# Optimization experiments

Measured on AMD Instinct MI355X. Metric: run time of the kernel, lower is better.

Reference implementation:

```python
import jax, jax.numpy as jnp
import numpy as np

BETA = 0.25  # commitment loss coefficient


def setup_inputs() -> dict:
    key = jax.random.key(0)
    kx, kc = jax.random.split(key)
    # x: [B, T, D] latents; codebooks: [M, K, D] (equal K per level -> stacked)
    x = jax.random.normal(kx, (64, 1024, 256), dtype=jnp.float32)
    # small init akin to RandomUniform(-1/K, 1/K)
    codebooks = jax.random.normal(kc, (4, 1024, 256), dtype=jnp.float32) * (1.0 / 1024.0)
    return {"x": x, "codebooks": codebooks}


def reference(x, codebooks):
    """Residual VQ forward (inference path: no EMA state update).

    Returns (y, commit_loss): y = x + stop_grad(sum_l q_l - x) (straight-through),
    commit_loss = beta * sum_l mean((stop_grad(q_l) - r_l)^2).
    """
    D = x.shape[-1]
    M = codebooks.shape[0]
    flat = x.reshape(-1, D)                      # [N, D]
    residual = flat
    q_sum = jnp.zeros_like(flat)
    commit = jnp.zeros((), dtype=x.dtype)
    for lvl in range(M):                         # M is small & fixed (4)
        cb = codebooks[lvl]                      # [K, D]
        # squared L2 distances: ||r||^2 + ||e||^2 - 2 r.e^T
        r2 = jnp.sum(residual * residual, axis=1, keepdims=True)   # [N, 1]
        e2 = jnp.sum(cb * cb, axis=1)                               # [K]
        dist = r2 + e2 - 2.0 * jnp.matmul(residual, cb.T)           # [N, K]
        idx = jnp.argmin(dist, axis=1)                              # [N]
        q = jnp.take(cb, idx, axis=0)                               # [N, D]
        q_st = jax.lax.stop_gradient(q)
        commit = commit + BETA * jnp.mean((q_st - residual) ** 2)
        q_sum = q_sum + q
        residual = residual - q_st
    y_flat = flat + jax.lax.stop_gradient(q_sum - flat)
    return y_flat.reshape(x.shape), commit
```

## Files before the change

kernel.cpp:

```cpp
#include <hip/hip_runtime.h>

#define DIM 256
#define KCODES 1024
#define LEVELS 4
#define CHUNK 64
#define NCHUNK 16
#define TOKB 128
#define NTOK 65536
#define NELEM (NTOK * DIM)

typedef _Float16 h8 __attribute__((ext_vector_type(8)));
typedef _Float16 h4 __attribute__((ext_vector_type(4)));
typedef _Float16 h2 __attribute__((ext_vector_type(2)));
typedef float f4 __attribute__((ext_vector_type(4)));
typedef unsigned int u32;

__device__ __forceinline__ void gload16(const void* g, void* l) {
  __builtin_amdgcn_global_load_lds(
      (const __attribute__((address_space(1))) void*)g,
      (__attribute__((address_space(3))) void*)l, 16, 0, 0);
}

__device__ __forceinline__ float sq8(h8 r, float acc) {
#if __has_builtin(__builtin_amdgcn_fdot2)
  #pragma unroll
  for (int j = 0; j < 4; ++j) {
    h2 p = {r[2 * j], r[2 * j + 1]};
    acc = __builtin_amdgcn_fdot2(p, p, acc, false);
  }
#else
  #pragma unroll
  for (int j = 0; j < 8; ++j) { float v = (float)r[j]; acc += v * v; }
#endif
  return acc;
}

__global__ __launch_bounds__(256) void rvq_prep(const float* __restrict__ cb,
                                                _Float16* __restrict__ cb16,
                                                float* __restrict__ e2p,
                                                float* __restrict__ out) {
  if (blockIdx.x == 0 && threadIdx.x == 0) out[NELEM] = 0.0f;
  const int row = blockIdx.x * 4 + (threadIdx.x >> 6);
  const int lane = threadIdx.x & 63;
  const float* src = cb + (size_t)row * DIM + lane * 4;
  f4 v = *(const f4*)src;
  h4 hv;
  hv[0] = (_Float16)v[0]; hv[1] = (_Float16)v[1];
  hv[2] = (_Float16)v[2]; hv[3] = (_Float16)v[3];
  *(h4*)(cb16 + (size_t)row * DIM + lane * 4) = hv;
  float s = v[0]*v[0] + v[1]*v[1] + v[2]*v[2] + v[3]*v[3];
  #pragma unroll
  for (int off = 32; off; off >>= 1) s += __shfl_xor(s, off, 64);
  if (lane == 0) e2p[row] = 0.25f - 0.5f * s;
}

__global__ __launch_bounds__(256, 2) void rvq_main(
    const float* __restrict__ x, const float* __restrict__ cb32,
    const _Float16* __restrict__ cb16, const float* __restrict__ e2p,
    float* __restrict__ out) {
  __shared__ __attribute__((aligned(16))) _Float16 clds[2][CHUNK * DIM];
  __shared__ float e2_lds[KCODES];
  __shared__ __attribute__((aligned(16))) int idx_hist[TOKB][4];
  __shared__ float r2_sh[TOKB];
  __shared__ float csum_sh[4];

  const int tid = threadIdx.x;
  const int wave = tid >> 6, lane = tid & 63;
  const int col = lane & 15, quad = lane >> 4;
  const int Llo = lane & 31, Lhi = lane >> 5;

  int soff[8], rdoff[8];
  #pragma unroll
  for (int i = 0; i < 8; ++i) {
    const int rl = wave * 16 + 2 * i + Lhi;
    soff[i] = rl * 512 + ((Llo ^ (rl & 7)) << 4);
  }
  #pragma unroll
  for (int kk = 0; kk < 8; ++kk)
    rdoff[kk] = (((kk * 4 + quad) ^ (col & 7)) << 4);

  const char* cb16b = (const char*)cb16;
  {
    char* ldst = (char*)&clds[0][0] + wave * 8192;
    #pragma unroll
    for (int i = 0; i < 8; ++i) gload16(cb16b + soff[i], ldst + i * 1024);
  }

  h8 af[2][8];
  float r2p[2] = {0.f, 0.f};
  const size_t tok0 = (size_t)blockIdx.x * TOKB + wave * 32;
  #pragma unroll
  for (int mt = 0; mt < 2; ++mt) {
    const float* xr = x + (tok0 + mt * 16 + col) * DIM + quad * 8;
    #pragma unroll
    for (int kk = 0; kk < 8; ++kk) {
      f4 a = *(const f4*)(xr + kk * 32);
      f4 b = *(const f4*)(xr + kk * 32 + 4);
      h8 h;
      #pragma unroll
      for (int j = 0; j < 4; ++j) { h[j] = (_Float16)a[j]; h[4 + j] = (_Float16)b[j]; }
      af[mt][kk] = h;
      r2p[mt] = sq8(h, r2p[mt]);
    }
  }

  float commit_acc = 0.f;

  for (int lvl = 0; lvl < LEVELS; ++lvl) {
    #pragma unroll
    for (int mt = 0; mt < 2; ++mt) {
      float s = r2p[mt];
      s += __shfl_xor(s, 16, 64);
      s += __shfl_xor(s, 32, 64);
      if (quad == 0) r2_sh[wave * 32 + mt * 16 + col] = s;
    }
    *(f4*)&e2_lds[tid * 4] = *(const f4*)(e2p + (lvl << 10) + tid * 4);

    u32 best[2][4];
    #pragma unroll
    for (int mt = 0; mt < 2; ++mt)
      #pragma unroll
      for (int i = 0; i < 4; ++i) best[mt][i] = 0u;

    for (int c = 0; c < NCHUNK; ++c) {
      __syncthreads();
      {
        const int gn = lvl * NCHUNK + c + 1;
        const char* gsrc = cb16b + ((size_t)(gn < 64 ? gn : 63) << 15);
        char* ldst = (char*)&clds[(c + 1) & 1][0] + wave * 8192;
        #pragma unroll
        for (int i = 0; i < 8; ++i) gload16(gsrc + soff[i], ldst + i * 1024);
      }

      const char* cbuf = (const char*)&clds[c & 1][0];
      #pragma unroll
      for (int nt = 0; nt < 4; ++nt) {
        const int code0 = c * 64 + nt * 16;
        const float e2v = e2_lds[code0 + col];
        f4 acc0 = {e2v, e2v, e2v, e2v};
        f4 acc1 = acc0;
        const char* bptr = cbuf + (nt * 16 + col) * 512;
        #pragma unroll
        for (int kk = 0; kk < 8; ++kk) {
          h8 b = *(const h8*)(bptr + rdoff[kk]);
          acc0 = __builtin_amdgcn_mfma_f32_16x16x32_f16(af[0][kk], b, acc0, 0, 0, 0);
          acc1 = __builtin_amdgcn_mfma_f32_16x16x32_f16(af[1][kk], b, acc1, 0, 0, 0);
        }
        const u32 invc = (u32)(code0 + col) ^ 1023u;
        #pragma unroll
        for (int i = 0; i < 4; ++i) {
          u32 p0 = (__float_as_uint(acc0[i]) & 0xFFFFFC00u) | invc;
          if (p0 > best[0][i]) best[0][i] = p0;
          u32 p1 = (__float_as_uint(acc1[i]) & 0xFFFFFC00u) | invc;
          if (p1 > best[1][i]) best[1][i] = p1;
        }
      }
    }

    #pragma unroll
    for (int mt = 0; mt < 2; ++mt)
      #pragma unroll
      for (int i = 0; i < 4; ++i) {
        u32 b = best[mt][i];
        #pragma unroll
        for (int off = 1; off < 16; off <<= 1) {
          u32 o = __shfl_xor(b, off, 16);
          if (o > b) b = o;
        }
        best[mt][i] = b;
      }

    if (col == 0) {
      #pragma unroll
      for (int mt = 0; mt < 2; ++mt)
        #pragma unroll
        for (int i = 0; i < 4; ++i) {
          const u32 p = best[mt][i];
          const int code = (int)((p & 1023u) ^ 1023u);
          const int t = wave * 32 + mt * 16 + quad * 4 + i;
          idx_hist[t][lvl] = code;
          const float sc = __uint_as_float(p & 0xFFFFFC00u) - 0.25f;
          commit_acc += r2_sh[t] - 2.0f * sc;
        }
    }
    __syncthreads();

    if (lvl < LEVELS - 1) {
      r2p[0] = 0.f; r2p[1] = 0.f;
      #pragma unroll
      for (int mt = 0; mt < 2; ++mt) {
        const int qidx = idx_hist[wave * 32 + mt * 16 + col][lvl];
        const _Float16* qr = cb16 + (((size_t)lvl << 10) + qidx) * DIM + quad * 8;
        #pragma unroll
        for (int kk = 0; kk < 8; ++kk) {
          h8 q = *(const h8*)(qr + kk * 32);
          h8 r = af[mt][kk] - q;
          af[mt][kk] = r;
          r2p[mt] = sq8(r, r2p[mt]);
        }
      }
    }
  }

  float* yblk = out + (size_t)blockIdx.x * (TOKB * DIM);
  #pragma unroll 4
  for (int it = 0; it < 32; ++it) {
    const int f = it * 1024 + tid * 4;
    const int t = f >> 8;
    const int d = f & 255;
    const int4 qi = *(const int4*)&idx_hist[t][0];
    f4 q0 = *(const f4*)(cb32 + (size_t)qi.x * DIM + d);
    f4 q1 = *(const f4*)(cb32 + (size_t)(1024 + qi.y) * DIM + d);
    f4 q2 = *(const f4*)(cb32 + (size_t)(2048 + qi.z) * DIM + d);
    f4 q3 = *(const f4*)(cb32 + (size_t)(3072 + qi.w) * DIM + d);
    f4 y = (q0 + q1) + (q2 + q3);
    *(f4*)(yblk + f) = y;
  }

  #pragma unroll
  for (int off = 1; off < 64; off <<= 1) commit_acc += __shfl_xor(commit_acc, off, 64);
  if (lane == 0) csum_sh[wave] = commit_acc;
  __syncthreads();
  if (tid == 0) {
    const float tot = csum_sh[0] + csum_sh[1] + csum_sh[2] + csum_sh[3];
    atomicAdd(out + NELEM, tot * (0.25f / 16777216.0f));
  }
}

extern "C" void kernel_launch(void* const* d_in, const int* in_sizes, int n_in,
                              void* d_out, int out_size, void* d_ws, size_t ws_size,
                              hipStream_t stream) {
  const float* x = (const float*)d_in[0];
  const float* cb = (const float*)d_in[1];
  float* out = (float*)d_out;
  _Float16* cb16 = (_Float16*)d_ws;
  float* e2p = (float*)((char*)d_ws + (size_t)LEVELS * KCODES * DIM * sizeof(_Float16));

  rvq_prep<<<(LEVELS * KCODES) / 4, 256, 0, stream>>>(cb, cb16, e2p, out);
  rvq_main<<<NTOK / TOKB, 256, 0, stream>>>(x, cb, cb16, e2p, out);
}
```

Baseline: 246.2 us.

## Switch distance GEMM to 32x32x16 MFMA with two waves per block

Replaces the 16x16x32 MFMA tiles with 32x32x16 tiles. Each wave now covers 64 tokens against 32-code tiles, and the block shrinks to 128 threads (2 waves) over the same 128 tokens. The goal is to cut LDS reads of the codebook per MFMA and raise per-wave arithmetic intensity. In exchange it holds many more registers (32 A fragments, 32-wide accumulators, 32 best values), uses launch bounds of 1 block, and gives fewer waves per CU to hide latency. The argmin reduction and the index/layout bookkeeping are reworked for the 32x32 output layout.

```diff
diff --git a/kernel.cpp b/kernel.cpp
--- a/kernel.cpp
+++ b/kernel.cpp
@@ -13,6 +13,7 @@
 typedef _Float16 h4 __attribute__((ext_vector_type(4)));
 typedef _Float16 h2 __attribute__((ext_vector_type(2)));
 typedef float f4 __attribute__((ext_vector_type(4)));
+typedef float fx16 __attribute__((ext_vector_type(16)));
 typedef unsigned int u32;
 
 __device__ __forceinline__ void gload16(const void* g, void* l) {
@@ -54,48 +55,46 @@
   if (lane == 0) e2p[row] = 0.25f - 0.5f * s;
 }
 
-__global__ __launch_bounds__(256, 2) void rvq_main(
+__global__ __launch_bounds__(128, 1) void rvq_main(
     const float* __restrict__ x, const float* __restrict__ cb32,
     const _Float16* __restrict__ cb16, const float* __restrict__ e2p,
     float* __restrict__ out) {
   __shared__ __attribute__((aligned(16))) _Float16 clds[2][CHUNK * DIM];
-  __shared__ float e2_lds[KCODES];
+  __shared__ __attribute__((aligned(16))) float e2_lds[KCODES];
   __shared__ __attribute__((aligned(16))) int idx_hist[TOKB][4];
   __shared__ float r2_sh[TOKB];
-  __shared__ float csum_sh[4];
+  __shared__ float csum_sh[2];
 
   const int tid = threadIdx.x;
   const int wave = tid >> 6, lane = tid & 63;
-  const int col = lane & 15, quad = lane >> 4;
   const int Llo = lane & 31, Lhi = lane >> 5;
 
-  int soff[8], rdoff[8];
-  #pragma unroll
-  for (int i = 0; i < 8; ++i) {
-    const int rl = wave * 16 + 2 * i + Lhi;
-    soff[i] = rl * 512 + ((Llo ^ (rl & 7)) << 4);
-  }
-  #pragma unroll
-  for (int kk = 0; kk < 8; ++kk)
-    rdoff[kk] = (((kk * 4 + quad) ^ (col & 7)) << 4);
+  int s4[4], rd4[4];
+  #pragma unroll
+  for (int j = 0; j < 4; ++j) {
+    const int key = (2 * j + Lhi) & 7;
+    s4[j] = (wave * 32 + 2 * j + Lhi) * 512 + ((Llo ^ key) << 4);
+    rd4[j] = (key ^ (Llo & 7)) << 4;
+  }
 
   const char* cb16b = (const char*)cb16;
   {
-    char* ldst = (char*)&clds[0][0] + wave * 8192;
-    #pragma unroll
-    for (int i = 0; i < 8; ++i) gload16(cb16b + soff[i], ldst + i * 1024);
-  }
-
-  h8 af[2][8];
+    char* ldst = (char*)&clds[0][0] + wave * 16384;
+    #pragma unroll
+    for (int i = 0; i < 16; ++i)
+      gload16(cb16b + s4[i & 3] + (i >> 2) * 4096, ldst + i * 1024);
+  }
+
+  h8 af[2][16];
   float r2p[2] = {0.f, 0.f};
-  const size_t tok0 = (size_t)blockIdx.x * TOKB + wave * 32;
+  const size_t tok0 = (size_t)blockIdx.x * TOKB + wave * 64;
   #pragma unroll
   for (int mt = 0; mt < 2; ++mt) {
-    const float* xr = x + (tok0 + mt * 16 + col) * DIM + quad * 8;
-    #pragma unroll
-    for (int kk = 0; kk < 8; ++kk) {
-      f4 a = *(const f4*)(xr + kk * 32);
-      f4 b = *(const f4*)(xr + kk * 32 + 4);
+    const float* xr = x + (tok0 + mt * 32 + Llo) * DIM + Lhi * 8;
+    #pragma unroll
+    for (int kk = 0; kk < 16; ++kk) {
+      f4 a = *(const f4*)(xr + kk * 16);
+      f4 b = *(const f4*)(xr + kk * 16 + 4);
       h8 h;
       #pragma unroll
       for (int j = 0; j < 4; ++j) { h[j] = (_Float16)a[j]; h[4 + j] = (_Float16)b[j]; }
@@ -109,46 +108,47 @@
   for (int lvl = 0; lvl < LEVELS; ++lvl) {
     #pragma unroll
     for (int mt = 0; mt < 2; ++mt) {
-      float s = r2p[mt];
-      s += __shfl_xor(s, 16, 64);
-      s += __shfl_xor(s, 32, 64);
-      if (quad == 0) r2_sh[wave * 32 + mt * 16 + col] = s;
-    }
-    *(f4*)&e2_lds[tid * 4] = *(const f4*)(e2p + (lvl << 10) + tid * 4);
-
-    u32 best[2][4];
+      float s = r2p[mt] + __shfl_xor(r2p[mt], 32, 64);
+      if (Lhi == 0) r2_sh[wave * 64 + mt * 32 + Llo] = s;
+    }
+    *(f4*)&e2_lds[tid * 8] = *(const f4*)(e2p + (lvl << 10) + tid * 8);
+    *(f4*)&e2_lds[tid * 8 + 4] = *(const f4*)(e2p + (lvl << 10) + tid * 8 + 4);
+
+    u32 best[2][16];
     #pragma unroll
     for (int mt = 0; mt < 2; ++mt)
       #pragma unroll
-      for (int i = 0; i < 4; ++i) best[mt][i] = 0u;
+      for (int i = 0; i < 16; ++i) best[mt][i] = 0u;
 
     for (int c = 0; c < NCHUNK; ++c) {
       __syncthreads();
       {
         const int gn = lvl * NCHUNK + c + 1;
         const char* gsrc = cb16b + ((size_t)(gn < 64 ? gn : 63) << 15);
-        char* ldst = (char*)&clds[(c + 1) & 1][0] + wave * 8192;
-        #pragma unroll
-        for (int i = 0; i < 8; ++i) gload16(gsrc + soff[i], ldst + i * 1024);
+        char* ldst = (char*)&clds[(c + 1) & 1][0] + wave * 16384;
+        #pragma unroll
+        for (int i = 0; i < 16; ++i)
+          gload16(gsrc + s4[i & 3] + (i >> 2) * 4096, ldst + i * 1024);
       }
 
       const char* cbuf = (const char*)&clds[c & 1][0];
       #pragma unroll
-      for (int nt = 0; nt < 4; ++nt) {
-        const int code0 = c * 64 + nt * 16;
-        const float e2v = e2_lds[code0 + col];
-        f4 acc0 = {e2v, e2v, e2v, e2v};
-        f4 acc1 = acc0;
-        const char* bptr = cbuf + (nt * 16 + col) * 512;
-        #pragma unroll
-        for (int kk = 0; kk < 8; ++kk) {
-          h8 b = *(const h8*)(bptr + rdoff[kk]);
-          acc0 = __builtin_amdgcn_mfma_f32_16x16x32_f16(af[0][kk], b, acc0, 0, 0, 0);
-          acc1 = __builtin_amdgcn_mfma_f32_16x16x32_f16(af[1][kk], b, acc1, 0, 0, 0);
-        }
-        const u32 invc = (u32)(code0 + col) ^ 1023u;
-        #pragma unroll
-        for (int i = 0; i < 4; ++i) {
+      for (int nt = 0; nt < 2; ++nt) {
+        const int code0 = c * 64 + nt * 32;
+        const float e2v = e2_lds[code0 + Llo];
+        fx16 acc0, acc1;
+        #pragma unroll
+        for (int i = 0; i < 16; ++i) { acc0[i] = e2v; acc1[i] = e2v; }
+        const char* bptr = cbuf + (nt * 32 + Llo) * 512;
+        #pragma unroll
+        for (int kk = 0; kk < 16; ++kk) {
+          h8 b = *(const h8*)(bptr + rd4[kk & 3] + (kk >> 2) * 128);
+          acc0 = __builtin_amdgcn_mfma_f32_32x32x16_f16(af[0][kk], b, acc0, 0, 0, 0);
+          acc1 = __builtin_amdgcn_mfma_f32_32x32x16_f16(af[1][kk], b, acc1, 0, 0, 0);
+        }
+        const u32 invc = ((u32)(code0 + Llo)) ^ 1023u;
+        #pragma unroll
+        for (int i = 0; i < 16; ++i) {
           u32 p0 = (__float_as_uint(acc0[i]) & 0xFFFFFC00u) | invc;
           if (p0 > best[0][i]) best[0][i] = p0;
           u32 p1 = (__float_as_uint(acc1[i]) & 0xFFFFFC00u) | invc;
@@ -160,24 +160,24 @@
     #pragma unroll
     for (int mt = 0; mt < 2; ++mt)
       #pragma unroll
-      for (int i = 0; i < 4; ++i) {
+      for (int i = 0; i < 16; ++i) {
         u32 b = best[mt][i];
         #pragma unroll
-        for (int off = 1; off < 16; off <<= 1) {
-          u32 o = __shfl_xor(b, off, 16);
+        for (int off = 1; off < 32; off <<= 1) {
+          u32 o = __shfl_xor(b, off, 32);
           if (o > b) b = o;
         }
         best[mt][i] = b;
       }
 
-    if (col == 0) {
+    if (Llo == 0) {
       #pragma unroll
       for (int mt = 0; mt < 2; ++mt)
         #pragma unroll
-        for (int i = 0; i < 4; ++i) {
+        for (int i = 0; i < 16; ++i) {
           const u32 p = best[mt][i];
           const int code = (int)((p & 1023u) ^ 1023u);
-          const int t = wave * 32 + mt * 16 + quad * 4 + i;
+          const int t = wave * 64 + mt * 32 + (i & 3) + 8 * (i >> 2) + 4 * Lhi;
           idx_hist[t][lvl] = code;
           const float sc = __uint_as_float(p & 0xFFFFFC00u) - 0.25f;
           commit_acc += r2_sh[t] - 2.0f * sc;
@@ -189,11 +189,11 @@
       r2p[0] = 0.f; r2p[1] = 0.f;
       #pragma unroll
       for (int mt = 0; mt < 2; ++mt) {
-        const int qidx = idx_hist[wave * 32 + mt * 16 + col][lvl];
-        const _Float16* qr = cb16 + (((size_t)lvl << 10) + qidx) * DIM + quad * 8;
-        #pragma unroll
-        for (int kk = 0; kk < 8; ++kk) {
-          h8 q = *(const h8*)(qr + kk * 32);
+        const int qidx = idx_hist[wave * 64 + mt * 32 + Llo][lvl];
+        const _Float16* qr = cb16 + (((size_t)lvl << 10) + qidx) * DIM + Lhi * 8;
+        #pragma unroll
+        for (int kk = 0; kk < 16; ++kk) {
+          h8 q = *(const h8*)(qr + kk * 16);
           h8 r = af[mt][kk] - q;
           af[mt][kk] = r;
           r2p[mt] = sq8(r, r2p[mt]);
@@ -204,8 +204,8 @@
 
   float* yblk = out + (size_t)blockIdx.x * (TOKB * DIM);
   #pragma unroll 4
-  for (int it = 0; it < 32; ++it) {
-    const int f = it * 1024 + tid * 4;
+  for (int it = 0; it < 64; ++it) {
+    const int f = it * 512 + tid * 4;
     const int t = f >> 8;
     const int d = f & 255;
     const int4 qi = *(const int4*)&idx_hist[t][0];
@@ -213,8 +213,8 @@
     f4 q1 = *(const f4*)(cb32 + (size_t)(1024 + qi.y) * DIM + d);
     f4 q2 = *(const f4*)(cb32 + (size_t)(2048 + qi.z) * DIM + d);
     f4 q3 = *(const f4*)(cb32 + (size_t)(3072 + qi.w) * DIM + d);
-    f4 y = (q0 + q1) + (q2 + q3);
-    *(f4*)(yblk + f) = y;
+    f4 yv = (q0 + q1) + (q2 + q3);
+    *(f4*)(yblk + f) = yv;
   }
 
   #pragma unroll
@@ -222,8 +222,7 @@
   if (lane == 0) csum_sh[wave] = commit_acc;
   __syncthreads();
   if (tid == 0) {
-    const float tot = csum_sh[0] + csum_sh[1] + csum_sh[2] + csum_sh[3];
-    atomicAdd(out + NELEM, tot * (0.25f / 16777216.0f));
+    atomicAdd(out + NELEM, (csum_sh[0] + csum_sh[1]) * (0.25f / 16777216.0f));
   }
 }
 
@@ -237,5 +236,5 @@
   float* e2p = (float*)((char*)d_ws + (size_t)LEVELS * KCODES * DIM * sizeof(_Float16));
 
   rvq_prep<<<(LEVELS * KCODES) / 4, 256, 0, stream>>>(cb, cb16, e2p, out);
-  rvq_main<<<NTOK / TOKB, 256, 0, stream>>>(x, cb, cb16, e2p, out);
-}
+  rvq_main<<<NTOK / TOKB, 128, 0, stream>>>(x, cb, cb16, e2p, out);
+}
```

Result: slower. 293.4 us (+19.2%).
